# Kernel optimization log

Hardware: AMD Instinct MI355X
Metric: run time of the kernel (lower is better)

Reference implementation:

```python
import jax, jax.numpy as jnp
import numpy as np
from jax import lax

BS, T, N, H = 32, 50, 192, 32


def setup_inputs() -> dict:
    key = jax.random.key(0)
    ks = jax.random.split(key, 30)
    w = lambda i, shape: jax.random.normal(ks[i], shape, dtype=jnp.float32) * 0.05
    return {
        "skill_seq": jax.random.randint(ks[0], (BS, T), 0, N),
        "adj": jax.random.uniform(ks[1], (1, BS, N, N), dtype=jnp.float32),
        "node_embeddings": w(2, (1, N, H)),
        "W_msg1": w(3, (H, 2 * H)), "b_msg1": w(4, (H,)),
        "W_msg2": w(5, (H, H)), "b_msg2": w(6, (H,)),
        "W_hr": w(7, (H, H)), "W_hi": w(8, (H, H)), "W_hh": w(9, (H, H)),
        "W_ir": w(10, (H, H)), "b_ir": w(11, (H,)),
        "W_ii": w(12, (H, H)), "b_ii": w(13, (H,)),
        "W_in": w(14, (H, H)), "b_in": w(15, (H,)),
        "W_o1": w(16, (H, H)), "b_o1": w(17, (H,)),
        "W_o2": w(18, (H, H)), "b_o2": w(19, (H,)),
        "W_o3": w(20, (H, H)), "b_o3": w(21, (H,)),
    }


def _forward(skill_seq, adj, node_embeddings,
             W_msg1, b_msg1, W_msg2, b_msg2,
             W_hr, W_hi, W_hh,
             W_ir, b_ir, W_ii, b_ii, W_in, b_in,
             W_o1, b_o1, W_o2, b_o2, W_o3, b_o3):
    bs, t_steps = skill_seq.shape
    n = adj.shape[-1]
    h = W_msg2.shape[0]
    lin = lambda x, W, b: x @ W.T + b
    # pre_msg = concat([senders, receivers], -1); split msg_fc1 accordingly so we
    # never materialize the [.., N*N, 2h] gather explicitly.
    W_send, W_recv = W_msg1[:, :h], W_msg1[:, h:]
    emb_seq = node_embeddings[0][skill_seq]            # [bs, T, h] (num_graph=1)
    xs = jnp.swapaxes(emb_seq[:, : t_steps - 1], 0, 1)  # [T-1, bs, h]
    hidden0 = jnp.zeros((1, bs, n, h), jnp.float32)     # leading graph dim = 1

    def step(hidden, x_t):
        send_p = hidden @ W_send.T                      # [1,bs,N,h]
        recv_p = hidden @ W_recv.T                      # [1,bs,N,h]
        # edge messages over all N*N (receiver, sender) pairs
        msg = jnp.tanh(recv_p[:, :, :, None, :] + send_p[:, :, None, :, :] + b_msg1)  # [1,bs,Nr,Ns,h]
        msg = jnp.tanh(lin(msg, W_msg2, b_msg2))
        # relation-masked scatter-sum over senders, normalized by num_nodes
        agg = jnp.einsum('gbrsh,gbrs->gbrh', msg, adj) / n  # [1,bs,N,h]
        inp = x_t[None, :, None, :]                     # [1,bs,1,h]
        r = jax.nn.sigmoid(lin(inp, W_ir, b_ir) + agg @ W_hr.T)
        i = jax.nn.sigmoid(lin(inp, W_ii, b_ii) + agg @ W_hi.T)
        nst = jnp.tanh(lin(inp, W_in, b_in) + r * (agg @ W_hh.T))
        hidden = (1.0 - i) * nst + i * hidden           # [1,bs,N,h]
        pred = jax.nn.relu(lin(hidden, W_o1, b_o1))     # dropout p=0 -> identity
        pred = jax.nn.relu(lin(pred, W_o2, b_o2))
        pred = lin(pred, W_o3, b_o3)
        return hidden, pred

    _, preds = lax.scan(step, hidden0, xs)              # [T-1,1,bs,N,h]
    # torch: stack(dim=1) -> [1,T-1,bs,N,h]; transpose(1,2) -> [1,bs,T-1,N,h]
    return jnp.transpose(preds, (1, 2, 0, 3, 4))


def reference(skill_seq, adj, node_embeddings,
              W_msg1, b_msg1, W_msg2, b_msg2,
              W_hr, W_hi, W_hh,
              W_ir, b_ir, W_ii, b_ii, W_in, b_in,
              W_o1, b_o1, W_o2, b_o2, W_o3, b_o3):
    return _forward(skill_seq, adj, node_embeddings,
                    W_msg1, b_msg1, W_msg2, b_msg2,
                    W_hr, W_hi, W_hh,
                    W_ir, b_ir, W_ii, b_ii, W_in, b_in,
                    W_o1, b_o1, W_o2, b_o2, W_o3, b_o3)
```

## Files before the change

### kernel.cpp

```cpp
#include <hip/hip_runtime.h>
#include <hip/hip_bf16.h>

#define BSZ 32
#define TT 50
#define NN 192
#define HH 32
#define NSTEP (TT - 1)
#define NODES_PER_BLK 8
#define BLKS_PER_B (NN / NODES_PER_BLK)
#define NBLK (BSZ * BLKS_PER_B)

#define BSLAB_F16 8192
#define SLAB_F16 (BSZ * BSLAB_F16)

typedef __attribute__((ext_vector_type(8))) short bf16x8;
typedef __attribute__((ext_vector_type(8))) _Float16 f16x8;
typedef __attribute__((ext_vector_type(2))) _Float16 f16x2;
typedef __attribute__((ext_vector_type(4))) float f32x4;

#define MFMA16(A, B, C) __builtin_amdgcn_mfma_f32_16x16x32_bf16((A), (B), (C), 0, 0, 0)
#define MFMAH(A, B, C)  __builtin_amdgcn_mfma_f32_16x16x32_f16((A), (B), (C), 0, 0, 0)

#define C2 2.885390081777927f

#if defined(__has_builtin)
#if __has_builtin(__builtin_amdgcn_exp2f)
#define EXP2(x) __builtin_amdgcn_exp2f(x)
#endif
#endif
#ifndef EXP2
#define EXP2(x) __expf(0.69314718056f * (x))
#endif

__device__ __forceinline__ float fast_rcp(float x) { return __builtin_amdgcn_rcpf(x); }
__device__ __forceinline__ float relu(float x) { return x > 0.0f ? x : 0.0f; }

__device__ __forceinline__ float tanh9(float x) {
    x = fminf(1.2f, fmaxf(-1.2f, x));
    float u = x * x;
    float h = __builtin_fmaf(u, 0.0090878f, -0.0447732f);
    h = __builtin_fmaf(u, h, 0.1302534f);
    h = __builtin_fmaf(u, h, -0.3329694f);
    h = __builtin_fmaf(u, h, 1.0000104f);
    return x * h;
}
__device__ __forceinline__ float sigmoid9(float x) {
    return __builtin_fmaf(0.5f, tanh9(0.5f * x), 0.5f);
}

__device__ __forceinline__ f16x2 splat2(float v) {
    f16x2 r; r[0] = (_Float16)v; r[1] = (_Float16)v; return r;
}
__device__ __forceinline__ f16x2 tanh9h2(f16x2 x) {
    x = __builtin_elementwise_min(__builtin_elementwise_max(x, splat2(-1.2f)), splat2(1.2f));
    f16x2 u = x * x;
    f16x2 h = __builtin_elementwise_fma(u, splat2(0.0090878f), splat2(-0.0447732f));
    h = __builtin_elementwise_fma(u, h, splat2(0.1302534f));
    h = __builtin_elementwise_fma(u, h, splat2(-0.3329694f));
    h = __builtin_elementwise_fma(u, h, splat2(1.0000104f));
    return x * h;
}

union U8 { bf16x8 v; __hip_bfloat162 p[4]; };
union UH { f16x8 v; f16x2 p[4]; };

__device__ __forceinline__ void ld8(const float* p, float* x) {
    const float4* q = (const float4*)p;
    float4 a = q[0], c = q[1];
    x[0] = a.x; x[1] = a.y; x[2] = a.z; x[3] = a.w;
    x[4] = c.x; x[5] = c.y; x[6] = c.z; x[7] = c.w;
}
__device__ __forceinline__ f16x8 packh8(const float* x) {
    UH u;
#pragma unroll
    for (int i = 0; i < 8; ++i) u.v[i] = (_Float16)x[i];
    return u.v;
}
__device__ __forceinline__ void split8(const float* x, bf16x8& hi, bf16x8& lo) {
    U8 H, L;
#pragma unroll
    for (int i = 0; i < 4; ++i) {
        __hip_bfloat162 h = __float22bfloat162_rn(make_float2(x[2 * i], x[2 * i + 1]));
        float2 hf = __bfloat1622float2(h);
        H.p[i] = h;
        L.p[i] = __float22bfloat162_rn(make_float2(x[2 * i] - hf.x, x[2 * i + 1] - hf.y));
    }
    hi = H.v; lo = L.v;
}
__device__ __forceinline__ void loadB_hl(const float* Wrow, bf16x8& h, bf16x8& l) {
    float x[8];
    ld8(Wrow, x);
    split8(x, h, l);
}

__global__ __launch_bounds__(512, 6) void k_all(
    const int* __restrict__ skill, const float* __restrict__ adj,
    const float* __restrict__ emb,
    const float* __restrict__ Wmsg1, const float* __restrict__ bmsg1,
    const float* __restrict__ Wmsg2, const float* __restrict__ bmsg2,
    const float* __restrict__ W_hr, const float* __restrict__ W_hi, const float* __restrict__ W_hh,
    const float* __restrict__ W_ir, const float* __restrict__ b_ir,
    const float* __restrict__ W_ii, const float* __restrict__ b_ii,
    const float* __restrict__ W_in, const float* __restrict__ b_in,
    _Float16* __restrict__ sbuf, unsigned* __restrict__ cnt, float* __restrict__ hist)
{
    __shared__ alignas(16) _Float16 spsh[NN][40];
    __shared__ alignas(16) float adjsh[8][NN];
    __shared__ alignas(16) float aggsh[16][36];
    __shared__ alignas(16) float hnsh[16][36];
    __shared__ alignas(16) float rvsh[8][36];
    __shared__ alignas(16) _Float16 ssh[8][32];
    __shared__ float grsh[8][33], gish[8][33], gnsh[8][33], ggsh[8][33];

    const int tid = threadIdx.x;
    const int w = tid >> 6, lane = tid & 63;
    const int n16 = lane & 15, kg = lane >> 4, k8 = kg * 8;
    const int m = blockIdx.x;
    const int b = (m & 7) * 4 + (m >> 3) / BLKS_PER_B;
    const int grp = (m >> 3) % BLKS_PER_B;
    const int node0 = b * NN + grp * NODES_PER_BLK;
    const int node = node0 + w;
    const int prod = w >> 1, hf = w & 1;
    const int rowb = hf * 16 + n16;

    for (int i = tid; i < 16 * 36; i += 512) { ((float*)aggsh)[i] = 0.f; ((float*)hnsh)[i] = 0.f; }
    for (int i = tid; i < 8 * 36; i += 512) ((float*)rvsh)[i] = 0.f;
    float A0w;
    {
        const float* ar = adj + (size_t)node * NN;
        float a0 = ar[lane], a1 = ar[lane + 64], a2v = ar[lane + 128];
        adjsh[w][lane] = a0; adjsh[w][lane + 64] = a1; adjsh[w][lane + 128] = a2v;
        float s = a0 + a1 + a2v;
#pragma unroll
        for (int mm = 1; mm < 64; mm <<= 1) s += __shfl_xor(s, mm, 64);
        A0w = s;
    }
    float b1r[8];
    ld8(bmsg1 + k8, b1r);
    f16x8 Bh0, Bh1;
    {
        float x[8];
        ld8(Wmsg2 + (size_t)n16 * HH + k8, x);
#pragma unroll
        for (int i = 0; i < 8; ++i) x[i] *= C2;
        Bh0 = packh8(x);
        ld8(Wmsg2 + (size_t)(16 + n16) * HH + k8, x);
#pragma unroll
        for (int i = 0; i < 8; ++i) x[i] *= C2;
        Bh1 = packh8(x);
    }
    const float cb2_0 = C2 * bmsg2[n16], cb2_1 = C2 * bmsg2[16 + n16];

    bf16x8 F0h{}, F0l{}, F1h{}, F1l{}, G0h{}, G0l{};
    float bias1 = 0.f;
    if (prod == 0) {
        loadB_hl(W_hr + (size_t)rowb * HH + k8, F0h, F0l);
        loadB_hl(W_ir + (size_t)rowb * HH + k8, F1h, F1l);
        bias1 = b_ir[rowb];
        loadB_hl(Wmsg1 + (size_t)rowb * 2 * HH + k8, G0h, G0l);
    } else if (prod == 1) {
        loadB_hl(W_hi + (size_t)rowb * HH + k8, F0h, F0l);
        loadB_hl(W_ii + (size_t)rowb * HH + k8, F1h, F1l);
        bias1 = b_ii[rowb];
        loadB_hl(Wmsg1 + (size_t)rowb * 2 * HH + HH + k8, G0h, G0l);
    } else if (prod == 2) {
        loadB_hl(W_in + (size_t)rowb * HH + k8, F0h, F0l);
        bias1 = b_in[rowb];
    } else {
        loadB_hl(W_hh + (size_t)rowb * HH + k8, F0h, F0l);
    }
    __syncthreads();

    for (int t = 0; t < NSTEP; ++t) {
        {
            const f16x8* src = (const f16x8*)(sbuf + (size_t)t * SLAB_F16 + (size_t)b * BSLAB_F16);
            f16x8 v0 = src[tid];
            *(f16x8*)&spsh[tid >> 2][(tid & 3) * 8] = v0;
            if (tid < 256) {
                const int c = tid + 512;
                f16x8 v1 = src[c];
                *(f16x8*)&spsh[c >> 2][(c & 3) * 8] = v1;
            }
        }
        UH rv;
        {
            float x[8];
            ld8(&rvsh[w][k8], x);
#pragma unroll
            for (int i = 0; i < 8; ++i) rv.v[i] = (_Float16)(x[i] + b1r[i]);
        }
        __syncthreads();

        float acc0 = 0.f, acc1 = 0.f;
#pragma unroll 2
        for (int s0 = 0; s0 < NN; s0 += 16) {
            UH a, tv;
            a.v = *(const f16x8*)&spsh[s0 + n16][k8];
#pragma unroll
            for (int i = 0; i < 4; ++i)
                tv.p[i] = tanh9h2(a.p[i] + rv.p[i]);
            f32x4 c0 = MFMAH(tv.v, Bh0, ((f32x4){cb2_0, cb2_0, cb2_0, cb2_0}));
            f32x4 c1 = MFMAH(tv.v, Bh1, ((f32x4){cb2_1, cb2_1, cb2_1, cb2_1}));
            const float4 a2 = *(const float4*)&adjsh[w][s0 + 4 * kg];
            acc0 = __builtin_fmaf(a2.x, fast_rcp(1.f + EXP2(c0[0])), acc0);
            acc0 = __builtin_fmaf(a2.y, fast_rcp(1.f + EXP2(c0[1])), acc0);
            acc0 = __builtin_fmaf(a2.z, fast_rcp(1.f + EXP2(c0[2])), acc0);
            acc0 = __builtin_fmaf(a2.w, fast_rcp(1.f + EXP2(c0[3])), acc0);
            acc1 = __builtin_fmaf(a2.x, fast_rcp(1.f + EXP2(c1[0])), acc1);
            acc1 = __builtin_fmaf(a2.y, fast_rcp(1.f + EXP2(c1[1])), acc1);
            acc1 = __builtin_fmaf(a2.z, fast_rcp(1.f + EXP2(c1[2])), acc1);
            acc1 = __builtin_fmaf(a2.w, fast_rcp(1.f + EXP2(c1[3])), acc1);
        }
        acc0 += __shfl_xor(acc0, 16, 64); acc0 += __shfl_xor(acc0, 32, 64);
        acc1 += __shfl_xor(acc1, 16, 64); acc1 += __shfl_xor(acc1, 32, 64);
        if (kg == 0) {
            aggsh[w][n16]      = (A0w - 2.f * acc0) * (1.0f / (float)NN);
            aggsh[w][16 + n16] = (A0w - 2.f * acc1) * (1.0f / (float)NN);
        }
        __syncthreads();

        {
            bf16x8 Agh{}, Agl{}, Aih{}, Ail{};
            if (prod != 2) { float x[8]; ld8(&aggsh[n16][k8], x); split8(x, Agh, Agl); }
            if (prod <= 2) {
                float x[8];
                const float* er = emb + (size_t)skill[b * TT + t] * HH;
                ld8(er + k8, x); split8(x, Aih, Ail);
            }
            f32x4 C = {bias1, bias1, bias1, bias1};
            if (prod <= 1) {
                C = MFMA16(Agh, F0h, C); C = MFMA16(Agh, F0l, C); C = MFMA16(Agl, F0h, C);
                C = MFMA16(Aih, F1h, C); C = MFMA16(Aih, F1l, C); C = MFMA16(Ail, F1h, C);
            } else if (prod == 2) {
                C = MFMA16(Aih, F0h, C); C = MFMA16(Aih, F0l, C); C = MFMA16(Ail, F0h, C);
            } else {
                C = MFMA16(Agh, F0h, C); C = MFMA16(Agh, F0l, C); C = MFMA16(Agl, F0h, C);
            }
            float* dst = (prod == 0) ? &grsh[0][0] : (prod == 1) ? &gish[0][0]
                       : (prod == 2) ? &gnsh[0][0] : &ggsh[0][0];
            if (kg < 2) {
#pragma unroll
                for (int j = 0; j < 4; ++j) dst[(4 * kg + j) * 33 + rowb] = C[j];
            }
        }
        __syncthreads();

        if (tid < 256) {
            const int row = tid >> 5, h = tid & 31;
            const float rg = sigmoid9(grsh[row][h]);
            const float ig = sigmoid9(gish[row][h]);
            const float ns = tanh9(gnsh[row][h] + rg * ggsh[row][h]);
            const float hn = (1.f - ig) * ns + ig * hnsh[row][h];
            hnsh[row][h] = hn;
            hist[(size_t)t * (BSZ * NN * HH) + (size_t)(node0 + row) * HH + h] = hn;
        }
        __syncthreads();

        if (w < 4) {
            const int p2 = w >> 1;
            bf16x8 Hh, Hl; float x[8];
            ld8(&hnsh[n16][k8], x); split8(x, Hh, Hl);
            f32x4 C = {0.f, 0.f, 0.f, 0.f};
            C = MFMA16(Hh, G0h, C); C = MFMA16(Hh, G0l, C); C = MFMA16(Hl, G0h, C);
            if (kg < 2) {
                if (p2 == 0) {
#pragma unroll
                    for (int j = 0; j < 4; ++j) ssh[4 * kg + j][rowb] = (_Float16)C[j];
                } else {
#pragma unroll
                    for (int j = 0; j < 4; ++j) rvsh[4 * kg + j][rowb] = C[j];
                }
            }
        }

        if (t < NSTEP - 1) {
            __syncthreads();
            _Float16* dstb = sbuf + (size_t)(t + 1) * SLAB_F16 + (size_t)b * BSLAB_F16
                           + (size_t)grp * (NODES_PER_BLK * HH);
            if (tid < 32) {
                f16x8 v = *(const f16x8*)&ssh[tid >> 2][(tid & 3) * 8];
                unsigned long long ad = (unsigned long long)dstb + (unsigned long long)tid * 16ull;
                asm volatile("global_store_dwordx4 %0, %1, off sc1" :: "v"(ad), "v"(v) : "memory");
            }
            if (tid == 0) {
                asm volatile("s_waitcnt vmcnt(0)" ::: "memory");
                __hip_atomic_fetch_add(&cnt[b * 16], 1u, __ATOMIC_RELAXED, __HIP_MEMORY_SCOPE_AGENT);
                const unsigned tgt = (unsigned)(BLKS_PER_B * (t + 1));
                while (__hip_atomic_load(&cnt[b * 16], __ATOMIC_RELAXED, __HIP_MEMORY_SCOPE_AGENT) < tgt)
                    __builtin_amdgcn_s_sleep(2);
            }
            __syncthreads();
        }
    }
}

#define CHUNK 8
__global__ __launch_bounds__(512, 6) void k_head(
    const float* __restrict__ hist,
    const float* __restrict__ W_o1, const float* __restrict__ b_o1,
    const float* __restrict__ W_o2, const float* __restrict__ b_o2,
    const float* __restrict__ W_o3, const float* __restrict__ b_o3,
    float* __restrict__ out)
{
    __shared__ alignas(16) float tsh[8][16][36];
    const int tid = threadIdx.x;
    const int w = tid >> 6, lane = tid & 63;
    const int n16 = lane & 15, kg = lane >> 4, k8 = kg * 8;

    bf16x8 W1h[2], W1l[2], W2h[2], W2l[2], W3h[2], W3l[2];
    float bb1[2], bb2[2], bb3[2];
#pragma unroll
    for (int hf = 0; hf < 2; ++hf) {
        const int rowb = hf * 16 + n16;
        loadB_hl(W_o1 + (size_t)rowb * HH + k8, W1h[hf], W1l[hf]); bb1[hf] = b_o1[rowb];
        loadB_hl(W_o2 + (size_t)rowb * HH + k8, W2h[hf], W2l[hf]); bb2[hf] = b_o2[rowb];
        loadB_hl(W_o3 + (size_t)rowb * HH + k8, W3h[hf], W3l[hf]); bb3[hf] = b_o3[rowb];
    }

    const int wgid = blockIdx.x * 8 + w;
#pragma unroll 1
    for (int c = 0; c < CHUNK; ++c) {
        const int cid = wgid * CHUNK + c;
        const int rc = cid % 12;
        const int tt = (cid / 12) % NSTEP;
        const int bb = cid / (12 * NSTEP);

        const float* hrow = hist + ((size_t)tt * BSZ * NN + (size_t)bb * NN + rc * 16) * HH;
        float x[8];
        bf16x8 Ah, Al;
        ld8(hrow + (size_t)n16 * HH + k8, x);
        split8(x, Ah, Al);

#pragma unroll
        for (int hf = 0; hf < 2; ++hf) {
            f32x4 C = {bb1[hf], bb1[hf], bb1[hf], bb1[hf]};
            C = MFMA16(Ah, W1h[hf], C); C = MFMA16(Ah, W1l[hf], C); C = MFMA16(Al, W1h[hf], C);
#pragma unroll
            for (int j = 0; j < 4; ++j) tsh[w][4 * kg + j][hf * 16 + n16] = relu(C[j]);
        }
        ld8(&tsh[w][n16][k8], x);
        split8(x, Ah, Al);

#pragma unroll
        for (int hf = 0; hf < 2; ++hf) {
            f32x4 C = {bb2[hf], bb2[hf], bb2[hf], bb2[hf]};
            C = MFMA16(Ah, W2h[hf], C); C = MFMA16(Ah, W2l[hf], C); C = MFMA16(Al, W2h[hf], C);
#pragma unroll
            for (int j = 0; j < 4; ++j) tsh[w][4 * kg + j][hf * 16 + n16] = relu(C[j]);
        }
        ld8(&tsh[w][n16][k8], x);
        split8(x, Ah, Al);

        float* obase = out + (((size_t)bb * NSTEP + tt) * NN + rc * 16) * HH;
#pragma unroll
        for (int hf = 0; hf < 2; ++hf) {
            f32x4 C = {bb3[hf], bb3[hf], bb3[hf], bb3[hf]};
            C = MFMA16(Ah, W3h[hf], C); C = MFMA16(Ah, W3l[hf], C); C = MFMA16(Al, W3h[hf], C);
#pragma unroll
            for (int j = 0; j < 4; ++j)
                obase[(size_t)(4 * kg + j) * HH + hf * 16 + n16] = C[j];
        }
    }
}

extern "C" void kernel_launch(void* const* d_in, const int* in_sizes, int n_in,
                              void* d_out, int out_size, void* d_ws, size_t ws_size,
                              hipStream_t stream) {
    const int*   skill = (const int*)d_in[0];
    const float* adj   = (const float*)d_in[1];
    const float* emb   = (const float*)d_in[2];
    const float* Wmsg1 = (const float*)d_in[3];
    const float* bmsg1 = (const float*)d_in[4];
    const float* Wmsg2 = (const float*)d_in[5];
    const float* bmsg2 = (const float*)d_in[6];
    const float* W_hr  = (const float*)d_in[7];
    const float* W_hi  = (const float*)d_in[8];
    const float* W_hh  = (const float*)d_in[9];
    const float* W_ir  = (const float*)d_in[10];
    const float* b_ir  = (const float*)d_in[11];
    const float* W_ii  = (const float*)d_in[12];
    const float* b_ii  = (const float*)d_in[13];
    const float* W_in  = (const float*)d_in[14];
    const float* b_in  = (const float*)d_in[15];
    const float* W_o1  = (const float*)d_in[16];
    const float* b_o1  = (const float*)d_in[17];
    const float* W_o2  = (const float*)d_in[18];
    const float* b_o2  = (const float*)d_in[19];
    const float* W_o3  = (const float*)d_in[20];
    const float* b_o3  = (const float*)d_in[21];
    float* out = (float*)d_out;

    char* base = (char*)d_ws;
    unsigned* cnt  = (unsigned*)base;
    _Float16* sbuf = (_Float16*)(base + 2048);
    float*    hist = (float*)(base + 2048 + (size_t)NSTEP * SLAB_F16 * 2);

    (void)hipMemsetAsync(d_ws, 0, 2048 + (size_t)SLAB_F16 * 2, stream);

    k_all<<<NBLK, 512, 0, stream>>>(
        skill, adj, emb, Wmsg1, bmsg1, Wmsg2, bmsg2,
        W_hr, W_hi, W_hh, W_ir, b_ir, W_ii, b_ii, W_in, b_in,
        sbuf, cnt, hist);

    k_head<<<294, 512, 0, stream>>>(hist, W_o1, b_o1, W_o2, b_o2, W_o3, b_o3, out);
}
```

Before: 966.8 us.

## Fuse output MLP head into recurrent kernel, drop hidden-history buffer

The three-layer output MLP now runs inside the recurrent kernel, on an otherwise idle wave (wave 7), each step right after the hidden state is updated. This removes the separate head kernel launch and the write and re-read of the full hidden-state history through global memory. The head work now sits in each step of the barrier-synchronised loop and reloads its weights from global memory every step. That may lengthen the critical path before the cross-block barrier if wave 7 finishes late. It also reuses the aggsh shared buffer as scratch, which relies on aggsh not being read again until the next step.

```diff
diff --git a/kernel.cpp b/kernel.cpp
--- a/kernel.cpp
+++ b/kernel.cpp
@@ -102,7 +102,10 @@
     const float* __restrict__ W_ir, const float* __restrict__ b_ir,
     const float* __restrict__ W_ii, const float* __restrict__ b_ii,
     const float* __restrict__ W_in, const float* __restrict__ b_in,
-    _Float16* __restrict__ sbuf, unsigned* __restrict__ cnt, float* __restrict__ hist)
+    const float* __restrict__ W_o1, const float* __restrict__ b_o1,
+    const float* __restrict__ W_o2, const float* __restrict__ b_o2,
+    const float* __restrict__ W_o3, const float* __restrict__ b_o3,
+    _Float16* __restrict__ sbuf, unsigned* __restrict__ cnt, float* __restrict__ out)
 {
     __shared__ alignas(16) _Float16 spsh[NN][40];
     __shared__ alignas(16) float adjsh[8][NN];
@@ -252,7 +255,6 @@
             const float ns = tanh9(gnsh[row][h] + rg * ggsh[row][h]);
             const float hn = (1.f - ig) * ns + ig * hnsh[row][h];
             hnsh[row][h] = hn;
-            hist[(size_t)t * (BSZ * NN * HH) + (size_t)(node0 + row) * HH + h] = hn;
         }
         __syncthreads();
 
@@ -272,16 +274,63 @@
                 }
             }
         }
-
-        if (t < NSTEP - 1) {
-            __syncthreads();
+        __syncthreads();
+
+        if (t < NSTEP - 1 && tid < 32) {
             _Float16* dstb = sbuf + (size_t)(t + 1) * SLAB_F16 + (size_t)b * BSLAB_F16
                            + (size_t)grp * (NODES_PER_BLK * HH);
-            if (tid < 32) {
-                f16x8 v = *(const f16x8*)&ssh[tid >> 2][(tid & 3) * 8];
-                unsigned long long ad = (unsigned long long)dstb + (unsigned long long)tid * 16ull;
-                asm volatile("global_store_dwordx4 %0, %1, off sc1" :: "v"(ad), "v"(v) : "memory");
-            }
+            f16x8 v = *(const f16x8*)&ssh[tid >> 2][(tid & 3) * 8];
+            unsigned long long ad = (unsigned long long)dstb + (unsigned long long)tid * 16ull;
+            asm volatile("global_store_dwordx4 %0, %1, off sc1" :: "v"(ad), "v"(v) : "memory");
+        }
+
+        if (w == 7) {
+            float x[8]; bf16x8 Ah, Al, Wh, Wl;
+            float (*tsh)[36] = aggsh;
+            ld8(&hnsh[n16][k8], x); split8(x, Ah, Al);
+#pragma unroll
+            for (int h2 = 0; h2 < 2; ++h2) {
+                const int rb = h2 * 16 + n16;
+                loadB_hl(W_o1 + (size_t)rb * HH + k8, Wh, Wl);
+                const float bb = b_o1[rb];
+                f32x4 C = {bb, bb, bb, bb};
+                C = MFMA16(Ah, Wh, C); C = MFMA16(Ah, Wl, C); C = MFMA16(Al, Wh, C);
+                if (kg < 2) {
+#pragma unroll
+                    for (int j = 0; j < 4; ++j) tsh[4 * kg + j][rb] = relu(C[j]);
+                }
+            }
+            ld8(&tsh[n16][k8], x); split8(x, Ah, Al);
+#pragma unroll
+            for (int h2 = 0; h2 < 2; ++h2) {
+                const int rb = h2 * 16 + n16;
+                loadB_hl(W_o2 + (size_t)rb * HH + k8, Wh, Wl);
+                const float bb = b_o2[rb];
+                f32x4 C = {bb, bb, bb, bb};
+                C = MFMA16(Ah, Wh, C); C = MFMA16(Ah, Wl, C); C = MFMA16(Al, Wh, C);
+                if (kg < 2) {
+#pragma unroll
+                    for (int j = 0; j < 4; ++j) tsh[4 * kg + j][rb] = relu(C[j]);
+                }
+            }
+            ld8(&tsh[n16][k8], x); split8(x, Ah, Al);
+            float* obase = out + (((size_t)b * NSTEP + t) * NN + grp * NODES_PER_BLK) * HH;
+#pragma unroll
+            for (int h2 = 0; h2 < 2; ++h2) {
+                const int rb = h2 * 16 + n16;
+                loadB_hl(W_o3 + (size_t)rb * HH + k8, Wh, Wl);
+                const float bb = b_o3[rb];
+                f32x4 C = {bb, bb, bb, bb};
+                C = MFMA16(Ah, Wh, C); C = MFMA16(Ah, Wl, C); C = MFMA16(Al, Wh, C);
+                if (kg < 2) {
+#pragma unroll
+                    for (int j = 0; j < 4; ++j)
+                        obase[(size_t)(4 * kg + j) * HH + rb] = C[j];
+                }
+            }
+        }
+
+        if (t < NSTEP - 1) {
             if (tid == 0) {
                 asm volatile("s_waitcnt vmcnt(0)" ::: "memory");
                 __hip_atomic_fetch_add(&cnt[b * 16], 1u, __ATOMIC_RELAXED, __HIP_MEMORY_SCOPE_AGENT);
@@ -290,75 +339,6 @@
                     __builtin_amdgcn_s_sleep(2);
             }
             __syncthreads();
-        }
-    }
-}
-
-#define CHUNK 8
-__global__ __launch_bounds__(512, 6) void k_head(
-    const float* __restrict__ hist,
-    const float* __restrict__ W_o1, const float* __restrict__ b_o1,
-    const float* __restrict__ W_o2, const float* __restrict__ b_o2,
-    const float* __restrict__ W_o3, const float* __restrict__ b_o3,
-    float* __restrict__ out)
-{
-    __shared__ alignas(16) float tsh[8][16][36];
-    const int tid = threadIdx.x;
-    const int w = tid >> 6, lane = tid & 63;
-    const int n16 = lane & 15, kg = lane >> 4, k8 = kg * 8;
-
-    bf16x8 W1h[2], W1l[2], W2h[2], W2l[2], W3h[2], W3l[2];
-    float bb1[2], bb2[2], bb3[2];
-#pragma unroll
-    for (int hf = 0; hf < 2; ++hf) {
-        const int rowb = hf * 16 + n16;
-        loadB_hl(W_o1 + (size_t)rowb * HH + k8, W1h[hf], W1l[hf]); bb1[hf] = b_o1[rowb];
-        loadB_hl(W_o2 + (size_t)rowb * HH + k8, W2h[hf], W2l[hf]); bb2[hf] = b_o2[rowb];
-        loadB_hl(W_o3 + (size_t)rowb * HH + k8, W3h[hf], W3l[hf]); bb3[hf] = b_o3[rowb];
-    }
-
-    const int wgid = blockIdx.x * 8 + w;
-#pragma unroll 1
-    for (int c = 0; c < CHUNK; ++c) {
-        const int cid = wgid * CHUNK + c;
-        const int rc = cid % 12;
-        const int tt = (cid / 12) % NSTEP;
-        const int bb = cid / (12 * NSTEP);
-
-        const float* hrow = hist + ((size_t)tt * BSZ * NN + (size_t)bb * NN + rc * 16) * HH;
-        float x[8];
-        bf16x8 Ah, Al;
-        ld8(hrow + (size_t)n16 * HH + k8, x);
-        split8(x, Ah, Al);
-
-#pragma unroll
-        for (int hf = 0; hf < 2; ++hf) {
-            f32x4 C = {bb1[hf], bb1[hf], bb1[hf], bb1[hf]};
-            C = MFMA16(Ah, W1h[hf], C); C = MFMA16(Ah, W1l[hf], C); C = MFMA16(Al, W1h[hf], C);
-#pragma unroll
-            for (int j = 0; j < 4; ++j) tsh[w][4 * kg + j][hf * 16 + n16] = relu(C[j]);
-        }
-        ld8(&tsh[w][n16][k8], x);
-        split8(x, Ah, Al);
-
-#pragma unroll
-        for (int hf = 0; hf < 2; ++hf) {
-            f32x4 C = {bb2[hf], bb2[hf], bb2[hf], bb2[hf]};
-            C = MFMA16(Ah, W2h[hf], C); C = MFMA16(Ah, W2l[hf], C); C = MFMA16(Al, W2h[hf], C);
-#pragma unroll
-            for (int j = 0; j < 4; ++j) tsh[w][4 * kg + j][hf * 16 + n16] = relu(C[j]);
-        }
-        ld8(&tsh[w][n16][k8], x);
-        split8(x, Ah, Al);
-
-        float* obase = out + (((size_t)bb * NSTEP + tt) * NN + rc * 16) * HH;
-#pragma unroll
-        for (int hf = 0; hf < 2; ++hf) {
-            f32x4 C = {bb3[hf], bb3[hf], bb3[hf], bb3[hf]};
-            C = MFMA16(Ah, W3h[hf], C); C = MFMA16(Ah, W3l[hf], C); C = MFMA16(Al, W3h[hf], C);
-#pragma unroll
-            for (int j = 0; j < 4; ++j)
-                obase[(size_t)(4 * kg + j) * HH + hf * 16 + n16] = C[j];
         }
     }
 }
@@ -393,14 +373,12 @@
     char* base = (char*)d_ws;
     unsigned* cnt  = (unsigned*)base;
     _Float16* sbuf = (_Float16*)(base + 2048);
-    float*    hist = (float*)(base + 2048 + (size_t)NSTEP * SLAB_F16 * 2);
 
     (void)hipMemsetAsync(d_ws, 0, 2048 + (size_t)SLAB_F16 * 2, stream);
 
     k_all<<<NBLK, 512, 0, stream>>>(
         skill, adj, emb, Wmsg1, bmsg1, Wmsg2, bmsg2,
         W_hr, W_hi, W_hh, W_ir, b_ir, W_ii, b_ii, W_in, b_in,
-        sbuf, cnt, hist);
-
-    k_head<<<294, 512, 0, stream>>>(hist, W_o1, b_o1, W_o2, b_o2, W_o3, b_o3, out);
-}
+        W_o1, b_o1, W_o2, b_o2, W_o3, b_o3,
+        sbuf, cnt, out);
+}
```

After: 1.184 ms. 22.5% more time.
